# Kernel tuning notes

Hardware: AMD Instinct MI355X
Metric: run time of the kernel (lower is better)

The kernel has to match this reference:

```python
import jax, jax.numpy as jnp
import numpy as np

NEG_BIG = -9e15
ALPHA = 0.2  # LeakyReLU slope


def setup_inputs() -> dict:
    key = jax.random.key(0)
    k1, k2, k3, k4 = jax.random.split(key, 4)
    B, N, Fin, Fout = 8, 2048, 256, 64
    h = jax.random.normal(k1, (B, N, Fin), dtype=jnp.float32)
    adj = jax.random.randint(k2, (B, N, N), 0, 2, dtype=jnp.int32)
    # xavier_uniform-ish scale for W and a
    W = jax.random.normal(k3, (Fin, Fout), dtype=jnp.float32) * (1.414 * np.sqrt(2.0 / (Fin + Fout)))
    a = jax.random.normal(k4, (2 * Fout, 1), dtype=jnp.float32) * (1.414 * np.sqrt(2.0 / (2 * Fout + 1)))
    return {"h": h, "adj": adj, "W": W, "a": a}


def reference(h, adj, W, a):
    Fout = W.shape[1]
    Wh = jnp.einsum("bnf,fo->bno", h, W)  # [B,N,Fout]
    # Decompose concat-based score: a_input @ a == Wh@a1 (src) + Wh@a2 (dst)
    a1, a2 = a[:Fout, 0], a[Fout:, 0]
    e_src = Wh @ a1  # [B,N]
    e_dst = Wh @ a2  # [B,N]
    e = e_src[:, :, None] + e_dst[:, None, :]  # [B,N,N]
    e = jnp.where(e > 0, e, ALPHA * e)  # LeakyReLU
    scores = jnp.where(adj > 0, e, NEG_BIG)
    attention = jax.nn.softmax(scores, axis=-1)  # [B,N,N]
    h_prime = jnp.einsum("bnm,bmo->bno", attention, Wh)
    return jax.nn.elu(h_prime)  # concat=True
```

## Files before the change

kernel.cpp:

```cpp
#include <hip/hip_runtime.h>

#define L2E 1.44269504088896340736f

typedef float f32x4 __attribute__((ext_vector_type(4)));
typedef __bf16 bf16x8 __attribute__((ext_vector_type(8)));
typedef __bf16 bf16x4 __attribute__((ext_vector_type(4)));

__device__ inline void mfma_bf16(bf16x8 a, bf16x8 b, f32x4& c) {
    c = __builtin_amdgcn_mfma_f32_16x16x32_bf16(a, b, c, 0, 0, 0);
}

#define WS_ESRC 2097152
#define WS_EDST 2162688
#define WS_NUM  2228224
#define WS_DEN  6422528


__global__ __launch_bounds__(256, 2)
void k1_wh(const float* __restrict__ h, const float* __restrict__ W,
           const float* __restrict__ a, __bf16* __restrict__ whP,
           float* __restrict__ esrc, float* __restrict__ edst,
           float* __restrict__ numden) {
    const int tid  = threadIdx.x;
    const int lane = tid & 63;
    const int w    = tid >> 6;
    const int blk  = blockIdx.x;
    const int r0   = blk * 8;
    const int b    = r0 >> 11;
    const int n0   = r0 & 2047;

    if (tid < 130) {
        const int zi = blk * 130 + tid;
        *(float4*)&numden[zi * 4] = make_float4(0.f, 0.f, 0.f, 0.f);
    }

    __shared__ float pt_s[8][4][64];
    __shared__ float whs[64][8];

    float wreg[64];
    {
        const float* Wp = W + (size_t)(w * 64) * 64 + lane;
#pragma unroll
        for (int kk = 0; kk < 64; kk++) wreg[kk] = Wp[(size_t)kk * 64];
    }

    const float* hbase = h + (size_t)r0 * 256 + w * 64;
    for (int rr = 0; rr < 8; rr++) {
        const float4* hp = (const float4*)(hbase + rr * 256);
        float acc = 0.f;
#pragma unroll
        for (int q = 0; q < 16; q++) {
            float4 hv = hp[q];
            acc += hv.x * wreg[4 * q + 0];
            acc += hv.y * wreg[4 * q + 1];
            acc += hv.z * wreg[4 * q + 2];
            acc += hv.w * wreg[4 * q + 3];
        }
        pt_s[rr][w][lane] = acc;
    }
    __syncthreads();

    const float a1 = a[lane];
    const float a2 = a[64 + lane];
#pragma unroll
    for (int rq = 0; rq < 2; rq++) {
        const int rr = w * 2 + rq;
        float v = pt_s[rr][0][lane] + pt_s[rr][1][lane] +
                  pt_s[rr][2][lane] + pt_s[rr][3][lane];
        whs[lane][rr] = v;
        float e1 = v * a1, e2 = v * a2;
#pragma unroll
        for (int d = 1; d < 64; d <<= 1) {
            e1 += __shfl_xor(e1, d);
            e2 += __shfl_xor(e2, d);
        }
        if (lane == 0) { esrc[r0 + rr] = e1; edst[r0 + rr] = e2; }
    }
    __syncthreads();

    if (tid < 128) {
        const int o  = tid >> 1, hf = (tid & 1) * 4;
        float4 v = *(const float4*)&whs[o][hf];
        bf16x4 bv = { (__bf16)v.x, (__bf16)v.y, (__bf16)v.z, (__bf16)v.w };
        const int t   = n0 >> 6;
        const int kh  = (n0 >> 5) & 1;
        const int hi2 = (n0 >> 3) & 3;
        const int ob  = o >> 4;
        const int rr  = o & 15;
        const size_t flat =
            ((((size_t)(b * 32 + t) * 2 + kh) * 4 + ob) * 4 + hi2) * 128 +
            rr * 8 + hf;
        *(bf16x4*)(whP + flat) = bv;
    }
}

__global__ __launch_bounds__(512, 4)
void k2_attn(const int* __restrict__ adj, const __bf16* __restrict__ whP,
             const float* __restrict__ esrc, const float* __restrict__ edst,
             float* __restrict__ num, float* __restrict__ den) {
    const int tid  = threadIdx.x;
    const int lane = tid & 63;
    const int w    = tid >> 6;
    const int blk  = blockIdx.x;
    const int b    = blk & 7;
    const int t2   = blk >> 3;
    const int jq   = t2 & 3;
    const int rg   = t2 >> 2;
    const int i0   = rg * 128;
    const int r    = lane & 15;
    const int hi   = lane >> 4;

    __shared__ __align__(16) __bf16 whp_s[32768];
    __shared__ float edst_s[512];
    __shared__ float esrc_s[128];
    __shared__ float red_s[8];

    const __bf16* wsrc = whP + (size_t)b * 131072 + (size_t)jq * 32768;
#pragma unroll
    for (int it = 0; it < 8; it++) {
        const int idx = it * 512 + tid;
        *(bf16x8*)&whp_s[idx * 8] = *(const bf16x8*)&wsrc[(size_t)idx * 8];
    }
    {
        float4 v = *(const float4*)&edst[b * 2048 + tid * 4];
        float mymax = fmaxf(fmaxf(v.x, v.y), fmaxf(v.z, v.w));
#pragma unroll
        for (int d = 1; d < 64; d <<= 1)
            mymax = fmaxf(mymax, __shfl_xor(mymax, d));
        if (lane == 0) red_s[w] = mymax;
    }
    edst_s[tid] = edst[b * 2048 + jq * 512 + tid];
    if (tid < 128) esrc_s[tid] = esrc[b * 2048 + i0 + tid];
    __syncthreads();

    float maxed = red_s[0];
#pragma unroll
    for (int q = 1; q < 8; q++) maxed = fmaxf(maxed, red_s[q]);
    const float es = esrc_s[w * 16 + r];
    float M = es + maxed;
    M = fmaxf(M, 0.2f * M);
    const float Mc = M * L2E;

    const int* arow = adj + (size_t)(b * 2048 + i0 + w * 16) * 2048 +
                      jq * 512 + lane;

    f32x4 lacc = {0.f, 0.f, 0.f, 0.f};
    f32x4 acc0 = {0,0,0,0}, acc1 = {0,0,0,0}, acc2 = {0,0,0,0}, acc3 = {0,0,0,0};

#define PB(E, bits, sh, base)                                                 \
    {                                                                         \
        const unsigned bb = (bits) >> (sh);                                   \
        float v;                                                              \
        v = es + E.x; v = fmaxf(v, 0.2f * v);                                 \
        p[base + 0] = (bb & 1u) ? exp2f(__builtin_fmaf(v, L2E, -Mc)) : 0.f;   \
        v = es + E.y; v = fmaxf(v, 0.2f * v);                                 \
        p[base + 1] = (bb & 2u) ? exp2f(__builtin_fmaf(v, L2E, -Mc)) : 0.f;   \
        v = es + E.z; v = fmaxf(v, 0.2f * v);                                 \
        p[base + 2] = (bb & 4u) ? exp2f(__builtin_fmaf(v, L2E, -Mc)) : 0.f;   \
        v = es + E.w; v = fmaxf(v, 0.2f * v);                                 \
        p[base + 3] = (bb & 8u) ? exp2f(__builtin_fmaf(v, L2E, -Mc)) : 0.f;   \
    }

    for (int tl = 0; tl < 8; ++tl) {
        const int jt = tl * 64;
        int av[16];
#pragma unroll
        for (int rr = 0; rr < 16; rr++) av[rr] = arow[(size_t)rr * 2048 + jt];
        const __bf16* wb = whp_s + tl * 4096 + lane * 8;
        bf16x8 B00 = *(const bf16x8*)(wb);
        bf16x8 B01 = *(const bf16x8*)(wb + 512);
        bf16x8 B02 = *(const bf16x8*)(wb + 1024);
        bf16x8 B03 = *(const bf16x8*)(wb + 1536);
        bf16x8 B10 = *(const bf16x8*)(wb + 2048);
        bf16x8 B11 = *(const bf16x8*)(wb + 2560);
        bf16x8 B12 = *(const bf16x8*)(wb + 3072);
        bf16x8 B13 = *(const bf16x8*)(wb + 3584);
        unsigned mlo = 0u, mhi2 = 0u;
#pragma unroll
        for (int rr = 0; rr < 16; rr++) {
            unsigned long long bal = __ballot(av[rr] > 0);
            if (r == rr) { mlo  = (unsigned)bal;
                           mhi2 = (unsigned)(bal >> 32); }
        }
        const unsigned aLo = mlo  >> (hi * 8);
        const unsigned aHi = mhi2 >> (hi * 8);
        float4 e0 = *(const float4*)&edst_s[jt + hi * 8];
        float4 e1 = *(const float4*)&edst_s[jt + hi * 8 + 4];
        float4 e2 = *(const float4*)&edst_s[jt + 32 + hi * 8];
        float4 e3 = *(const float4*)&edst_s[jt + 32 + hi * 8 + 4];
        float p[16];
        PB(e0, aLo, 0, 0) PB(e1, aLo, 4, 4) PB(e2, aHi, 0, 8) PB(e3, aHi, 4, 12)
        lacc[0] += p[0] + p[4] + p[8]  + p[12];
        lacc[1] += p[1] + p[5] + p[9]  + p[13];
        lacc[2] += p[2] + p[6] + p[10] + p[14];
        lacc[3] += p[3] + p[7] + p[11] + p[15];
        bf16x8 pa0, pa1;
#pragma unroll
        for (int e = 0; e < 8; e++) {
            pa0[e] = (__bf16)p[e];
            pa1[e] = (__bf16)p[e + 8];
        }
        mfma_bf16(pa0, B00, acc0); mfma_bf16(pa1, B10, acc0);
        mfma_bf16(pa0, B01, acc1); mfma_bf16(pa1, B11, acc1);
        mfma_bf16(pa0, B02, acc2); mfma_bf16(pa1, B12, acc2);
        mfma_bf16(pa0, B03, acc3); mfma_bf16(pa1, B13, acc3);
    }
#undef PB

    float lsum = lacc[0] + lacc[1] + lacc[2] + lacc[3];
    lsum += __shfl_xor(lsum, 16);
    lsum += __shfl_xor(lsum, 32);
    const int rowbase = b * 2048 + i0 + w * 16;
    if (lane < 16) atomicAdd(&den[rowbase + r], lsum);
#pragma unroll
    for (int reg = 0; reg < 4; reg++) {
        float* np = num + (size_t)(rowbase + 4 * hi + reg) * 64 + r;
        atomicAdd(np +  0, acc0[reg]);
        atomicAdd(np + 16, acc1[reg]);
        atomicAdd(np + 32, acc2[reg]);
        atomicAdd(np + 48, acc3[reg]);
    }
}

__global__ __launch_bounds__(256, 4)
void k3_fin(const float* __restrict__ num, const float* __restrict__ den,
            float* __restrict__ out) {
    const int i = blockIdx.x * 256 + threadIdx.x;
    float4 n = *(const float4*)&num[(size_t)i * 4];
    const float inv = 1.0f / den[i >> 4];
    float v0 = n.x * inv, v1 = n.y * inv, v2 = n.z * inv, v3 = n.w * inv;
    v0 = v0 > 0.f ? v0 : expm1f(v0);
    v1 = v1 > 0.f ? v1 : expm1f(v1);
    v2 = v2 > 0.f ? v2 : expm1f(v2);
    v3 = v3 > 0.f ? v3 : expm1f(v3);
    *(float4*)&out[(size_t)i * 4] = make_float4(v0, v1, v2, v3);
}

extern "C" void kernel_launch(void* const* d_in, const int* in_sizes, int n_in,
                              void* d_out, int out_size, void* d_ws, size_t ws_size,
                              hipStream_t stream) {
    const float* h   = (const float*)d_in[0];
    const int*   adj = (const int*)d_in[1];
    const float* W   = (const float*)d_in[2];
    const float* a   = (const float*)d_in[3];
    float* out = (float*)d_out;

    char* ws = (char*)d_ws;
    __bf16* whP  = (__bf16*)ws;
    float*  esrc = (float*)(ws + WS_ESRC);
    float*  edst = (float*)(ws + WS_EDST);
    float*  num  = (float*)(ws + WS_NUM);
    float*  den  = (float*)(ws + WS_DEN);

    hipLaunchKernelGGL(k1_wh, dim3(2048), dim3(256), 0, stream,
                       h, W, a, whP, esrc, edst, num);
    hipLaunchKernelGGL(k2_attn, dim3(512), dim3(512), 0, stream,
                       adj, whP, esrc, edst, num, den);
    hipLaunchKernelGGL(k3_fin, dim3(1024), dim3(256), 0, stream,
                       num, den, out);
}
```

Baseline: 73.06 us.

## Pre-pack adjacency into bitmask kernel and stage mask tiles in shared memory

Adds a separate kernel that reads the int32 adjacency matrix with wide vector loads and packs it into 32-bit bitmasks. The attention kernel then loads its mask tile into shared memory instead of doing strided per-row global loads and ballot reductions inside the main loop. This aims to get better-coalesced streaming of the 128MB adjacency and to shorten the inner loop. The cost is an extra kernel launch and a small mask write/read round trip, and the lowered occupancy hint trades waves for more LDS.

New measurement: 86.04 us. 1.18x slower.

```diff
diff --git a/kernel.cpp b/kernel.cpp
--- a/kernel.cpp
+++ b/kernel.cpp
@@ -14,7 +14,26 @@
 #define WS_EDST 2162688
 #define WS_NUM  2228224
 #define WS_DEN  6422528
-
+#define WS_MSK  6488064
+
+
+__global__ __launch_bounds__(256, 8)
+void k_msk(const int* __restrict__ adj, unsigned* __restrict__ mask) {
+    const int t = blockIdx.x * 256 + threadIdx.x;
+    const int4* ap = (const int4*)(adj + (size_t)t * 32);
+    int4 q0 = ap[0], q1 = ap[1], q2 = ap[2], q3 = ap[3];
+    int4 q4 = ap[4], q5 = ap[5], q6 = ap[6], q7 = ap[7];
+    unsigned m = 0u;
+#define PK(Q, S)                                                              \
+    m |= ((Q.x > 0) ? 1u : 0u) << (S);                                        \
+    m |= ((Q.y > 0) ? 1u : 0u) << ((S) + 1);                                  \
+    m |= ((Q.z > 0) ? 1u : 0u) << ((S) + 2);                                  \
+    m |= ((Q.w > 0) ? 1u : 0u) << ((S) + 3);
+    PK(q0, 0) PK(q1, 4) PK(q2, 8) PK(q3, 12)
+    PK(q4, 16) PK(q5, 20) PK(q6, 24) PK(q7, 28)
+#undef PK
+    mask[t] = m;
+}
 
 __global__ __launch_bounds__(256, 2)
 void k1_wh(const float* __restrict__ h, const float* __restrict__ W,
@@ -94,8 +113,8 @@
     }
 }
 
-__global__ __launch_bounds__(512, 4)
-void k2_attn(const int* __restrict__ adj, const __bf16* __restrict__ whP,
+__global__ __launch_bounds__(512, 2)
+void k2_attn(const unsigned* __restrict__ mask, const __bf16* __restrict__ whP,
              const float* __restrict__ esrc, const float* __restrict__ edst,
              float* __restrict__ num, float* __restrict__ den) {
     const int tid  = threadIdx.x;
@@ -111,6 +130,7 @@
     const int hi   = lane >> 4;
 
     __shared__ __align__(16) __bf16 whp_s[32768];
+    __shared__ unsigned msk_s[128][18];
     __shared__ float edst_s[512];
     __shared__ float esrc_s[128];
     __shared__ float red_s[8];
@@ -120,6 +140,14 @@
     for (int it = 0; it < 8; it++) {
         const int idx = it * 512 + tid;
         *(bf16x8*)&whp_s[idx * 8] = *(const bf16x8*)&wsrc[(size_t)idx * 8];
+    }
+    const unsigned* mbase = mask + (size_t)(b * 2048 + i0) * 64 + jq * 16;
+#pragma unroll
+    for (int it = 0; it < 4; it++) {
+        const int idx  = it * 512 + tid;
+        const int rloc = idx >> 4;
+        const int wloc = idx & 15;
+        msk_s[rloc][wloc] = mbase[(size_t)rloc * 64 + wloc];
     }
     {
         float4 v = *(const float4*)&edst[b * 2048 + tid * 4];
@@ -140,9 +168,6 @@
     float M = es + maxed;
     M = fmaxf(M, 0.2f * M);
     const float Mc = M * L2E;
-
-    const int* arow = adj + (size_t)(b * 2048 + i0 + w * 16) * 2048 +
-                      jq * 512 + lane;
 
     f32x4 lacc = {0.f, 0.f, 0.f, 0.f};
     f32x4 acc0 = {0,0,0,0}, acc1 = {0,0,0,0}, acc2 = {0,0,0,0}, acc3 = {0,0,0,0};
@@ -163,9 +188,9 @@
 
     for (int tl = 0; tl < 8; ++tl) {
         const int jt = tl * 64;
-        int av[16];
-#pragma unroll
-        for (int rr = 0; rr < 16; rr++) av[rr] = arow[(size_t)rr * 2048 + jt];
+        const uint2 m2 = *(const uint2*)&msk_s[w * 16 + r][tl * 2];
+        const unsigned aLo = m2.x >> (hi * 8);
+        const unsigned aHi = m2.y >> (hi * 8);
         const __bf16* wb = whp_s + tl * 4096 + lane * 8;
         bf16x8 B00 = *(const bf16x8*)(wb);
         bf16x8 B01 = *(const bf16x8*)(wb + 512);
@@ -175,15 +200,6 @@
         bf16x8 B11 = *(const bf16x8*)(wb + 2560);
         bf16x8 B12 = *(const bf16x8*)(wb + 3072);
         bf16x8 B13 = *(const bf16x8*)(wb + 3584);
-        unsigned mlo = 0u, mhi2 = 0u;
-#pragma unroll
-        for (int rr = 0; rr < 16; rr++) {
-            unsigned long long bal = __ballot(av[rr] > 0);
-            if (r == rr) { mlo  = (unsigned)bal;
-                           mhi2 = (unsigned)(bal >> 32); }
-        }
-        const unsigned aLo = mlo  >> (hi * 8);
-        const unsigned aHi = mhi2 >> (hi * 8);
         float4 e0 = *(const float4*)&edst_s[jt + hi * 8];
         float4 e1 = *(const float4*)&edst_s[jt + hi * 8 + 4];
         float4 e2 = *(const float4*)&edst_s[jt + 32 + hi * 8];
@@ -246,16 +262,18 @@
     float* out = (float*)d_out;
 
     char* ws = (char*)d_ws;
-    __bf16* whP  = (__bf16*)ws;
-    float*  esrc = (float*)(ws + WS_ESRC);
-    float*  edst = (float*)(ws + WS_EDST);
-    float*  num  = (float*)(ws + WS_NUM);
-    float*  den  = (float*)(ws + WS_DEN);
-
+    __bf16*   whP  = (__bf16*)ws;
+    float*    esrc = (float*)(ws + WS_ESRC);
+    float*    edst = (float*)(ws + WS_EDST);
+    float*    num  = (float*)(ws + WS_NUM);
+    float*    den  = (float*)(ws + WS_DEN);
+    unsigned* mask = (unsigned*)(ws + WS_MSK);
+
+    hipLaunchKernelGGL(k_msk, dim3(4096), dim3(256), 0, stream, adj, mask);
     hipLaunchKernelGGL(k1_wh, dim3(2048), dim3(256), 0, stream,
                        h, W, a, whP, esrc, edst, num);
     hipLaunchKernelGGL(k2_attn, dim3(512), dim3(512), 0, stream,
-                       adj, whP, esrc, edst, num, den);
+                       mask, whP, esrc, edst, num, den);
     hipLaunchKernelGGL(k3_fin, dim3(1024), dim3(256), 0, stream,
                        num, den, out);
 }
```
